# Kernel tuning notes

Hardware: AMD Instinct MI355X
Metric: run time of the kernel (lower is better)

Reference implementation:

```python
import jax, jax.numpy as jnp
import numpy as np

GRID_SIZE = 8
MARGIN = 1.0
EPS = 1e-8


def _centers_xy(hc, wc, gs):
    # pixel coordinates of cell centers for a hc x wc grid with stride gs, (x, y) order
    ys = jnp.arange(hc, dtype=jnp.float32) * gs + gs / 2.0 - 0.5
    xs = jnp.arange(wc, dtype=jnp.float32) * gs + gs / 2.0 - 0.5
    gy, gx = jnp.meshgrid(ys, xs, indexing='ij')
    return jnp.stack([gx, gy], axis=-1).reshape(-1, 2)  # (hc*wc, 2)


def _warp_xy(coords_xy, homo):
    # coords_xy: (n,2), homo: (b,3,3) -> (b,n,2) perspective warp
    p = jnp.concatenate([coords_xy, jnp.ones_like(coords_xy[..., :1])], axis=-1)  # (n,3)
    q = jnp.einsum('bij,nj->bni', homo, p)
    return q[..., :2] / (q[..., 2:3] + EPS)


def _bilinear(img, coords_yx):
    # img: (b,c,h,w); coords_yx: (b,n,2) pixel coords -> (b,n,c), zero padding outside
    b, c, h, w = img.shape
    y, x = coords_yx[..., 0], coords_yx[..., 1]
    y0, x0 = jnp.floor(y), jnp.floor(x)
    wy1, wx1 = y - y0, x - x0

    def gat(yi, xi):
        valid = (yi >= 0) & (yi <= h - 1) & (xi >= 0) & (xi <= w - 1)
        yc = jnp.clip(yi, 0, h - 1).astype(jnp.int32)
        xc = jnp.clip(xi, 0, w - 1).astype(jnp.int32)
        v = jax.vmap(lambda im, yy, xx: im[:, yy, xx].T)(img, yc, xc)  # (b,n,c)
        return v * valid[..., None].astype(img.dtype)

    return (gat(y0, x0) * ((1 - wy1) * (1 - wx1))[..., None]
            + gat(y0, x0 + 1) * ((1 - wy1) * wx1)[..., None]
            + gat(y0 + 1, x0) * (wy1 * (1 - wx1))[..., None]
            + gat(y0 + 1, x0 + 1) * (wy1 * wx1)[..., None])


def setup_inputs():
    key = jax.random.key(0)
    k = jax.random.split(key, 6)
    b, c, H, W = 2, 64, 480, 640
    hc, wc = H // GRID_SIZE, W // GRID_SIZE
    score1 = jax.random.uniform(k[0], (b, 1, H, W), dtype=jnp.float32)
    score2 = jax.random.uniform(k[1], (b, 1, H, W), dtype=jnp.float32)
    desc1 = jax.random.normal(k[2], (b, c, hc, wc), dtype=jnp.float32)
    desc1 = desc1 / jnp.linalg.norm(desc1, axis=1, keepdims=True)
    desc2 = jax.random.normal(k[3], (b, c, hc, wc), dtype=jnp.float32)
    desc2 = desc2 / jnp.linalg.norm(desc2, axis=1, keepdims=True)
    homo12 = jnp.eye(3, dtype=jnp.float32)[None] + 0.005 * jax.random.normal(k[4], (b, 3, 3), dtype=jnp.float32)
    homo21 = jnp.linalg.inv(homo12)
    return {"score1": score1, "score2": score2, "desc1": desc1, "desc2": desc2,
            "homo12": homo12, "homo21": homo21}


def reference(score1, score2, desc1, desc2, homo12, homo21):
    b, c, hc, wc = desc1.shape
    H, W = score1.shape[-2], score1.shape[-1]
    n = hc * wc
    gs = GRID_SIZE

    # warp image1 cell centers into image2 pixel space
    coo1_xy = _centers_xy(hc, wc, gs)                 # (n,2) x,y
    w_xy = _warp_xy(coo1_xy, homo12)                  # (b,n,2)
    w_yx = w_xy[..., ::-1]                            # (b,n,2) y,x

    # sample image2 descriptors at warped locations (desc-grid coordinates)
    d_yx = (w_yx - gs / 2.0 + 0.5) / gs
    w_desc1 = _bilinear(desc2, d_yx)                  # (b,n,c)
    w_desc1 = w_desc1 / (jnp.linalg.norm(w_desc1, axis=-1, keepdims=True) + EPS)

    # visibility: warp a ones image by homo21; keep only fully visible cells
    pix_xy = _centers_xy(H, W, 1)                     # (H*W,2)
    wp_xy = _warp_xy(pix_xy, homo21)                  # (b,HW,2)
    ones = jnp.ones((b, 1, H, W), desc1.dtype)
    vis = (_bilinear(ones, wp_xy[..., ::-1]) > 0).astype(desc1.dtype)  # (b,HW,1)
    vis = vis.reshape(b, 1, hc, gs, wc, gs).transpose(0, 3, 5, 1, 2, 4).reshape(b, gs * gs, hc, wc)
    w_vis_mask = jnp.prod(vis, axis=1).reshape(b, 1, n)

    # pairwise coordinate distances + 4-NN neighbor mask
    coo2_yx = _centers_xy(hc, wc, gs)[:, ::-1]        # (n,2) y,x
    a2 = jnp.sum(w_yx * w_yx, axis=-1)                # (b,n)
    b2 = jnp.sum(coo2_yx * coo2_yx, axis=-1)          # (n,)
    coo_dist = jnp.sqrt(jnp.clip(
        a2[:, :, None] + b2[None, None, :] - 2.0 * jnp.einsum('bnd,md->bnm', w_yx, coo2_yx), 0.0))
    _, ids = jax.lax.top_k(-coo_dist, 4)              # 4 smallest distances
    bi = jnp.arange(b)[:, None, None]
    ri = jnp.arange(n)[None, :, None]
    neigh_mask = jnp.zeros_like(coo_dist).at[bi, ri, ids].set(1.0)

    # descriptor inverse-similarity (euclidean distance of unit descriptors)
    d1 = desc1.reshape(b, c, n).transpose(0, 2, 1)    # (b,n,c)
    d2 = desc2.reshape(b, c, n).transpose(0, 2, 1)
    desc_sim = jnp.sqrt(jnp.clip(2.0 - 2.0 * jnp.einsum('bnc,bmc->bnm', d1, d2), EPS))
    desc_sim = desc_sim + neigh_mask * 5.0 + (1.0 - w_vis_mask) * 5.0

    # keypoints whose warps land inside image2
    in_b = ((w_yx[..., 0] >= 0) & (w_yx[..., 0] <= H - 1)
            & (w_yx[..., 1] >= 0) & (w_yx[..., 1] <= W - 1))
    match_mask = in_b.astype(desc1.dtype)             # (b,n)

    pos_sim = jnp.sqrt(jnp.clip(2.0 - 2.0 * jnp.sum(d1 * w_desc1, axis=-1), EPS))
    neg_sim = jnp.min(desc_sim, axis=-1)
    loss = jnp.clip(pos_sim - neg_sim + MARGIN, 0.0) ** 2
    return jnp.sum(loss * match_mask) / jnp.sum(match_mask)
```

## Files before the change

### kernel.cpp

```cpp
#include <hip/hip_runtime.h>
#include <math.h>

#define GS 8
#define HC 60
#define WC 80
#define NN 4800
#define CC 64
#define BB 2
#define HIMG 480
#define WIMG 640
#define EPSF 1e-8f
#define NCT 300
#define TGN 24
#define BIGF 1e30f

typedef __attribute__((ext_vector_type(8))) short short8v;
typedef __attribute__((ext_vector_type(4))) float f32x4;

__device__ __forceinline__ unsigned short f2bf(float f) {
    unsigned u = __float_as_uint(f);
    u += 0x7FFFu + ((u >> 16) & 1u);
    return (unsigned short)(u >> 16);
}

__global__ __launch_bounds__(256) void k_pre(
    const float* __restrict__ desc1, const float* __restrict__ desc2,
    const float* __restrict__ homo12, const float* __restrict__ homo21,
    unsigned short* __restrict__ d1bf, unsigned short* __restrict__ d2bf,
    float* __restrict__ posim, float* __restrict__ matchm,
    float* __restrict__ biasf, int* __restrict__ neighpk,
    unsigned int* __restrict__ negbits)
{
    __shared__ unsigned short tile[CC][65];
    int bid = blockIdx.x;
    int tid = threadIdx.x;

    if (bid < 2 * BB * 75) {
        int arr = bid / (BB * 75);
        int rem = bid % (BB * 75);
        int b = rem / 75;
        int t = rem % 75;
        int c0 = t * 64;
        const float* in = arr ? desc2 : desc1;
        unsigned short* out = arr ? d2bf : d1bf;
        int w = tid >> 6, l = tid & 63;
        #pragma unroll
        for (int k = 0; k < 16; k++) {
            int ch = k * 4 + w;
            tile[ch][l] = f2bf(in[((size_t)(b * CC + ch)) * NN + c0 + l]);
        }
        __syncthreads();
        #pragma unroll
        for (int k = 0; k < 16; k++) {
            int cell = k * 4 + w;
            out[((size_t)b * NN + c0 + cell) * CC + l] = tile[l][cell];
        }
        return;
    }

    int sub = bid - 2 * BB * 75;
    int wv = tid >> 6, lane = tid & 63;
    int idx = sub * 4 + wv;
    int b = idx / NN, r = idx - b * NN;
    int ci = r / WC, cj = r - ci * WC;

    int allv;
    {
        const float* h = homo21 + b * 9;
        int di = lane >> 3, dj = lane & 7;
        float y = (float)(ci * 8 + di);
        float x = (float)(cj * 8 + dj);
        float qx = h[0]*x + h[1]*y + h[2];
        float qy = h[3]*x + h[4]*y + h[5];
        float qw = h[6]*x + h[7]*y + h[8];
        float px = qx / (qw + EPSF);
        float py = qy / (qw + EPSF);
        float y0 = floorf(py), x0 = floorf(px);
        float ty = py - y0,   tx = px - x0;
        float fyv = ((y0 >= 0.0f && y0 <= (float)(HIMG-1)) ? (1.0f-ty) : 0.0f)
                  + ((y0+1.0f >= 0.0f && y0+1.0f <= (float)(HIMG-1)) ? ty : 0.0f);
        float fxv = ((x0 >= 0.0f && x0 <= (float)(WIMG-1)) ? (1.0f-tx) : 0.0f)
                  + ((x0+1.0f >= 0.0f && x0+1.0f <= (float)(WIMG-1)) ? tx : 0.0f);
        int ok = (fyv > 0.0f && fxv > 0.0f) ? 1 : 0;
        allv = __all(ok);
    }

    const float* h = homo12 + b * 9;
    float xx = cj * 8.0f + 3.5f;
    float yy = ci * 8.0f + 3.5f;
    float qx = h[0]*xx + h[1]*yy + h[2];
    float qy = h[3]*xx + h[4]*yy + h[5];
    float qw = h[6]*xx + h[7]*yy + h[8];
    float wx = qx / (qw + EPSF);
    float wy = qy / (qw + EPSF);
    float dy = (wy - 4.0f + 0.5f) / 8.0f;
    float dx = (wx - 4.0f + 0.5f) / 8.0f;

    float y0f = floorf(dy), x0f = floorf(dx);
    float fy = dy - y0f, fx = dx - x0f;
    float y1f = y0f + 1.0f, x1f = x0f + 1.0f;
    bool v0y = (y0f >= 0.0f && y0f <= (float)(HC-1));
    bool v1y = (y1f >= 0.0f && y1f <= (float)(HC-1));
    bool v0x = (x0f >= 0.0f && x0f <= (float)(WC-1));
    bool v1x = (x1f >= 0.0f && x1f <= (float)(WC-1));
    float w00 = (1.0f-fy)*(1.0f-fx); if (!(v0y && v0x)) w00 = 0.0f;
    float w01 = (1.0f-fy)*fx;        if (!(v0y && v1x)) w01 = 0.0f;
    float w10 = fy*(1.0f-fx);        if (!(v1y && v0x)) w10 = 0.0f;
    float w11 = fy*fx;               if (!(v1y && v1x)) w11 = 0.0f;
    int yc0 = (int)fminf(fmaxf(y0f, 0.0f), (float)(HC-1));
    int yc1 = (int)fminf(fmaxf(y1f, 0.0f), (float)(HC-1));
    int xc0 = (int)fminf(fmaxf(x0f, 0.0f), (float)(WC-1));
    int xc1 = (int)fminf(fmaxf(x1f, 0.0f), (float)(WC-1));
    int o00 = yc0*WC + xc0, o01 = yc0*WC + xc1;
    int o10 = yc1*WC + xc0, o11 = yc1*WC + xc1;

    int ch = lane;
    const float* d2b = desc2 + (size_t)b * CC * NN;
    const float* p = d2b + ch * NN;
    float wvl = w00*p[o00] + w01*p[o01] + w10*p[o10] + w11*p[o11];
    float s2 = wvl * wvl;
    float sd = desc1[((size_t)(b * CC + ch)) * NN + r] * wvl;
    #pragma unroll
    for (int off = 1; off < 64; off <<= 1) {
        s2 += __shfl_xor(s2, off);
        sd += __shfl_xor(sd, off);
    }

    if (lane == 0) {
        biasf[idx] = allv ? 16.0f : 8.0f;
        matchm[idx] = (wy >= 0.0f && wy <= (float)(HIMG-1) &&
                       wx >= 0.0f && wx <= (float)(WIMG-1)) ? 1.0f : 0.0f;
        float dot = sd / (sqrtf(s2) + EPSF);
        posim[idx] = sqrtf(fmaxf(2.0f - 2.0f*dot, EPSF));

        int i0 = (int)floorf(dy);
        int j0 = (int)floorf(dx);
        int ilo = i0 - 1; if (ilo < 0) ilo = 0; if (ilo > HC-4) ilo = HC-4;
        int jlo = j0 - 1; if (jlo < 0) jlo = 0; if (jlo > WC-4) jlo = WC-4;
        float bd0=3e38f, bd1=3e38f, bd2=3e38f, bd3=3e38f;
        int   id0=0,     id1=0,     id2=0,     id3=0;
        #pragma unroll
        for (int a = 0; a < 4; a++) {
            float cy = (float)(ilo + a) * 8.0f + 3.5f;
            float ddy = wy - cy;
            float ddy2 = ddy * ddy;
            #pragma unroll
            for (int q = 0; q < 4; q++) {
                float cx = (float)(jlo + q) * 8.0f + 3.5f;
                float ddx = wx - cx;
                float dv = ddy2 + ddx * ddx;
                int id = (ilo + a) * WC + (jlo + q);
                if (dv < bd3) {
                    bd3 = dv; id3 = id;
                    if (bd3 < bd2) { float tf=bd2; bd2=bd3; bd3=tf; int ti=id2; id2=id3; id3=ti; }
                    if (bd2 < bd1) { float tf=bd1; bd1=bd2; bd2=tf; int ti=id1; id1=id2; id2=ti; }
                    if (bd1 < bd0) { float tf=bd0; bd0=bd1; bd1=tf; int ti=id0; id0=id1; id1=ti; }
                }
            }
        }
        int base = ilo * WC + jlo;
        int mask = 0;
        {
            int d, ri, rj;
            d = id0 - base; ri = d / WC; rj = d - ri * WC; mask |= 1 << (ri*4+rj);
            d = id1 - base; ri = d / WC; rj = d - ri * WC; mask |= 1 << (ri*4+rj);
            d = id2 - base; ri = d / WC; rj = d - ri * WC; mask |= 1 << (ri*4+rj);
            d = id3 - base; ri = d / WC; rj = d - ri * WC; mask |= 1 << (ri*4+rj);
        }
        neighpk[idx] = mask | (ilo << 16) | (jlo << 24);
        negbits[idx] = 0x7F800000u;
    }
}


#define GLL(gp, lp) __builtin_amdgcn_global_load_lds(                        \
    (const __attribute__((address_space(1))) unsigned int*)(gp),             \
    (__attribute__((address_space(3))) unsigned int*)(lp), 16, 0, 0)

#define MFMA16(A, B, C) __builtin_amdgcn_mfma_f32_16x16x32_bf16((A), (B), (C), 0, 0, 0)

__global__ __launch_bounds__(64) void k_negmin(
    const unsigned short* __restrict__ d1bf, const unsigned short* __restrict__ d2bf,
    const float* __restrict__ biasf, const int* __restrict__ neighpk,
    unsigned int* __restrict__ negbits)
{
    __shared__ unsigned short Bsm[2][1024];

    int bid = blockIdx.x;
    int b   = bid / (150 * TGN);
    int rem = bid % (150 * TGN);
    int rb  = rem / TGN;
    int tg  = rem % TGN;
    int lane = threadIdx.x;
    int l15 = lane & 15, lg = lane >> 4;
    int r0  = rb * 32;
    int wl  = l15;
    int lg8 = lg * 8;
    int bNN = b * NN;

    const unsigned short* d1b = d1bf + (size_t)bNN * CC;
    const unsigned short* d2b = d2bf + (size_t)bNN * CC;

    short8v afr00 = *(const short8v*)(d1b + (size_t)(r0 + l15) * CC + lg8);
    short8v afr01 = *(const short8v*)(d1b + (size_t)(r0 + l15) * CC + 32 + lg8);
    short8v afr10 = *(const short8v*)(d1b + (size_t)(r0 + 16 + l15) * CC + lg8);
    short8v afr11 = *(const short8v*)(d1b + (size_t)(r0 + 16 + l15) * CC + 32 + lg8);

    int pk[8];
    int lmin = 0x7FFFFFFF, lmax = -1;
    #pragma unroll
    for (int s_ = 0; s_ < 8; s_++) {
        int row = r0 + (s_ >> 2) * 16 + lg * 4 + (s_ & 3);
        int p = neighpk[bNN + row];
        pk[s_] = p;
        int ilo = (p >> 16) & 0xFF, jlo = (p >> 24) & 0xFF;
        int idm = ilo * WC + jlo;
        lmin = min(lmin, idm);
        lmax = max(lmax, idm + 3 * WC + 3);
    }
    #pragma unroll
    for (int off = 1; off < 64; off <<= 1) {
        lmin = min(lmin, __shfl_xor(lmin, off));
        lmax = max(lmax, __shfl_xor(lmax, off));
    }

    float m[8];
    #pragma unroll
    for (int i = 0; i < 8; i++) m[i] = -BIGF;

    int o0 = lane;
    int o1 = lane + 64;
    int s0 = (o0 & ~7) | ((o0 ^ (o0 >> 3)) & 7);
    int s1 = (o1 & ~7) | ((o1 ^ (o1 >> 3)) & 7);

    int nt = (NCT - tg + TGN - 1) / TGN;

    {
        const unsigned short* tb0 = d2b + (size_t)(tg * 16) * CC;
        GLL(tb0 + s0 * 8, &Bsm[0][0]);
        GLL(tb0 + s1 * 8, &Bsm[0][512]);
    }
    float bias = biasf[bNN + tg * 16 + wl];
    __syncthreads();

    int buf = 0;
    for (int it = 0; it < nt; it++) {
        int t = tg + it * TGN;

        float bias_n = 0.0f;
        if (it + 1 < nt) {
            const unsigned short* tbn = d2b + (size_t)((t + TGN) * 16) * CC;
            GLL(tbn + s0 * 8, &Bsm[buf ^ 1][0]);
            GLL(tbn + s1 * 8, &Bsm[buf ^ 1][512]);
            bias_n = biasf[bNN + (t + TGN) * 16 + wl];
        }

        const unsigned short* lb = &Bsm[buf][0];
        short8v b0 = *(const short8v*)(lb + (size_t)wl * 64 + (size_t)((lg ^ wl) & 7) * 8);
        short8v b1 = *(const short8v*)(lb + (size_t)wl * 64 + (size_t)(((4 + lg) ^ wl) & 7) * 8);

        f32x4 a0 = {bias, bias, bias, bias};
        f32x4 a1 = a0;
        a0 = MFMA16(afr00, b0, a0);
        a0 = MFMA16(afr01, b1, a0);
        a1 = MFMA16(afr10, b0, a1);
        a1 = MFMA16(afr11, b1, a1);

        int tb = t * 16;
        if (tb + 15 < lmin || tb > lmax) {
            #pragma unroll
            for (int g_ = 0; g_ < 4; g_++) {
                m[g_]   = fmaxf(m[g_],   a0[g_]);
                m[4+g_] = fmaxf(m[4+g_], a1[g_]);
            }
        } else {
            int c_ = tb + wl;
            int gi_ = c_ / WC; int gj_ = c_ - gi_ * WC;
            #pragma unroll
            for (int s_ = 0; s_ < 8; s_++) {
                int p_ = pk[s_]; int msk_ = p_ & 0xFFFF;
                unsigned ri_ = (unsigned)(gi_ - ((p_ >> 16) & 0xFF));
                unsigned rj_ = (unsigned)(gj_ - ((p_ >> 24) & 0xFF));
                unsigned bx_ = (ri_ < 4u && rj_ < 4u) ? (ri_ * 4u + rj_) : 16u;
                bool nb_ = ((msk_ >> bx_) & 1) != 0;
                float sv_ = (s_ < 4) ? a0[s_ & 3] : a1[s_ & 3];
                float key_ = nb_ ? sv_ - 8.0f : sv_;
                m[s_] = fmaxf(m[s_], key_);
            }
        }

        bias = bias_n;
        buf ^= 1;
        __syncthreads();
    }

    #pragma unroll
    for (int s_ = 0; s_ < 8; s_++) {
        float mv = m[s_];
        float pen, sdot;
        if (mv >= 12.0f)     { pen = 0.0f;  sdot = mv - 16.0f; }
        else if (mv >= 4.0f) { pen = 5.0f;  sdot = mv - 8.0f; }
        else                 { pen = 10.0f; sdot = mv; }
        float res = sqrtf(fmaxf(2.0f - 2.0f * sdot, EPSF)) + pen;
        #pragma unroll
        for (int off = 1; off < 16; off <<= 1)
            res = fminf(res, __shfl_xor(res, off));
        if (l15 == 0) {
            int row = r0 + (s_ >> 2) * 16 + lg * 4 + (s_ & 3);
            atomicMin(&negbits[bNN + row], __float_as_uint(res));
        }
    }
}

__global__ void k_loss(const float* __restrict__ posim, const float* __restrict__ matchm,
                       const unsigned int* __restrict__ negbits, float* __restrict__ bpart)
{
    __shared__ float sn[256], sdn[256];
    int tid = threadIdx.x;
    int idx = blockIdx.x * 256 + tid;
    float num = 0.0f, den = 0.0f;
    if (idx < BB * NN) {
        float neg = __uint_as_float(negbits[idx]);
        float l = fmaxf(posim[idx] - neg + 1.0f, 0.0f);
        float mm = matchm[idx];
        num = l * l * mm;
        den = mm;
    }
    sn[tid] = num; sdn[tid] = den;
    __syncthreads();
    for (int st = 128; st > 0; st >>= 1) {
        if (tid < st) { sn[tid] += sn[tid + st]; sdn[tid] += sdn[tid + st]; }
        __syncthreads();
    }
    if (tid == 0) { bpart[blockIdx.x * 2] = sn[0]; bpart[blockIdx.x * 2 + 1] = sdn[0]; }
}

__global__ void k_sum(const float* __restrict__ bpart, int nb, float* __restrict__ out)
{
    int t = threadIdx.x;
    float num = 0.0f, den = 0.0f;
    if (t < nb) { num = bpart[t * 2]; den = bpart[t * 2 + 1]; }
    #pragma unroll
    for (int off = 1; off < 64; off <<= 1) {
        num += __shfl_xor(num, off);
        den += __shfl_xor(den, off);
    }
    if (t == 0) out[0] = num / den;
}

extern "C" void kernel_launch(void* const* d_in, const int* in_sizes, int n_in,
                              void* d_out, int out_size, void* d_ws, size_t ws_size,
                              hipStream_t stream)
{
    const float* desc1  = (const float*)d_in[2];
    const float* desc2  = (const float*)d_in[3];
    const float* homo12 = (const float*)d_in[4];
    const float* homo21 = (const float*)d_in[5];
    float* out = (float*)d_out;

    float*        biasf   = (float*)d_ws;
    float*        posim   = biasf + BB * NN;
    float*        matchm  = posim + BB * NN;
    int*          neighpk = (int*)(matchm + BB * NN);
    unsigned int* negbits = (unsigned int*)(neighpk + BB * NN);
    float*        bpart   = (float*)(negbits + BB * NN);
    unsigned short* d1bf  = (unsigned short*)(bpart + 128);
    unsigned short* d2bf  = d1bf + (size_t)BB * NN * CC;

    int nb = (BB * NN + 255) / 256;
    int nb_pre = 2 * BB * 75 + 2 * BB * 75 * 4;
    k_pre<<<nb_pre, 256, 0, stream>>>(desc1, desc2, homo12, homo21,
                                      d1bf, d2bf, posim, matchm, biasf, neighpk, negbits);
    k_negmin<<<BB * 150 * TGN, 64, 0, stream>>>(d1bf, d2bf, biasf, neighpk, negbits);
    k_loss<<<nb, 256, 0, stream>>>(posim, matchm, negbits, bpart);
    k_sum<<<1, 64, 0, stream>>>(bpart, nb, out);
}
```

Before: 38.76 us.

## Triple-buffer descriptor tiles with explicit vmcnt waits, staging bias through LDS

Replaces the double-buffered loop, which called __syncthreads every iteration, with a three-stage ring. Descriptor tiles and bias values are prefetched two iterations ahead using global_load_lds, and the loop waits on explicit s_waitcnt vmcnt counts instead of a barrier. Bias now moves through LDS via 4-byte DMA loads instead of per-lane register prefetch. This hides more global-load latency for the single-wave blocks, but it relies on hand-counted vmcnt values and uses extra LDS, so any miscount could read a tile before it has arrived.

```diff
diff --git a/kernel.cpp b/kernel.cpp
--- a/kernel.cpp
+++ b/kernel.cpp
@@ -173,9 +173,12 @@
 }
 
 
-#define GLL(gp, lp) __builtin_amdgcn_global_load_lds(                        \
+#define GLL16(gp, lp) __builtin_amdgcn_global_load_lds(                      \
     (const __attribute__((address_space(1))) unsigned int*)(gp),             \
     (__attribute__((address_space(3))) unsigned int*)(lp), 16, 0, 0)
+#define GLL4(gp, lp) __builtin_amdgcn_global_load_lds(                       \
+    (const __attribute__((address_space(1))) unsigned int*)(gp),             \
+    (__attribute__((address_space(3))) unsigned int*)(lp), 4, 0, 0)
 
 #define MFMA16(A, B, C) __builtin_amdgcn_mfma_f32_16x16x32_bf16((A), (B), (C), 0, 0, 0)
 
@@ -184,7 +187,8 @@
     const float* __restrict__ biasf, const int* __restrict__ neighpk,
     unsigned int* __restrict__ negbits)
 {
-    __shared__ unsigned short Bsm[2][1024];
+    __shared__ unsigned short Bsm[3][1024];
+    __shared__ float Bias[3][64];
 
     int bid = blockIdx.x;
     int b   = bid / (150 * TGN);
@@ -235,64 +239,64 @@
 
     int nt = (NCT - tg + TGN - 1) / TGN;
 
-    {
-        const unsigned short* tb0 = d2b + (size_t)(tg * 16) * CC;
-        GLL(tb0 + s0 * 8, &Bsm[0][0]);
-        GLL(tb0 + s1 * 8, &Bsm[0][512]);
-    }
-    float bias = biasf[bNN + tg * 16 + wl];
-    __syncthreads();
-
-    int buf = 0;
-    for (int it = 0; it < nt; it++) {
-        int t = tg + it * TGN;
-
-        float bias_n = 0.0f;
-        if (it + 1 < nt) {
-            const unsigned short* tbn = d2b + (size_t)((t + TGN) * 16) * CC;
-            GLL(tbn + s0 * 8, &Bsm[buf ^ 1][0]);
-            GLL(tbn + s1 * 8, &Bsm[buf ^ 1][512]);
-            bias_n = biasf[bNN + (t + TGN) * 16 + wl];
-        }
-
-        const unsigned short* lb = &Bsm[buf][0];
-        short8v b0 = *(const short8v*)(lb + (size_t)wl * 64 + (size_t)((lg ^ wl) & 7) * 8);
-        short8v b1 = *(const short8v*)(lb + (size_t)wl * 64 + (size_t)(((4 + lg) ^ wl) & 7) * 8);
-
-        f32x4 a0 = {bias, bias, bias, bias};
-        f32x4 a1 = a0;
-        a0 = MFMA16(afr00, b0, a0);
-        a0 = MFMA16(afr01, b1, a0);
-        a1 = MFMA16(afr10, b0, a1);
-        a1 = MFMA16(afr11, b1, a1);
-
-        int tb = t * 16;
-        if (tb + 15 < lmin || tb > lmax) {
-            #pragma unroll
-            for (int g_ = 0; g_ < 4; g_++) {
-                m[g_]   = fmaxf(m[g_],   a0[g_]);
-                m[4+g_] = fmaxf(m[4+g_], a1[g_]);
-            }
-        } else {
-            int c_ = tb + wl;
-            int gi_ = c_ / WC; int gj_ = c_ - gi_ * WC;
-            #pragma unroll
-            for (int s_ = 0; s_ < 8; s_++) {
-                int p_ = pk[s_]; int msk_ = p_ & 0xFFFF;
-                unsigned ri_ = (unsigned)(gi_ - ((p_ >> 16) & 0xFF));
-                unsigned rj_ = (unsigned)(gj_ - ((p_ >> 24) & 0xFF));
-                unsigned bx_ = (ri_ < 4u && rj_ < 4u) ? (ri_ * 4u + rj_) : 16u;
-                bool nb_ = ((msk_ >> bx_) & 1) != 0;
-                float sv_ = (s_ < 4) ? a0[s_ & 3] : a1[s_ & 3];
-                float key_ = nb_ ? sv_ - 8.0f : sv_;
-                m[s_] = fmaxf(m[s_], key_);
-            }
-        }
-
-        bias = bias_n;
-        buf ^= 1;
-        __syncthreads();
-    }
+#define STAGE(T, S) do {                                                     \
+    const unsigned short* tbp_ = d2b + (size_t)((T) * 16) * CC;              \
+    GLL16(tbp_ + s0 * 8, &Bsm[S][0]);                                        \
+    GLL16(tbp_ + s1 * 8, &Bsm[S][512]);                                      \
+    GLL4(biasf + bNN + (T) * 16 + l15, &Bias[S][0]);                         \
+} while (0)
+
+#define COMP(T, S) do {                                                      \
+    const unsigned short* lb_ = &Bsm[S][0];                                  \
+    short8v b0_ = *(const short8v*)(lb_ + (size_t)wl * 64 +                  \
+                                    (size_t)((lg ^ wl) & 7) * 8);            \
+    short8v b1_ = *(const short8v*)(lb_ + (size_t)wl * 64 +                  \
+                                    (size_t)(((4 + lg) ^ wl) & 7) * 8);      \
+    float bi_ = Bias[S][wl];                                                 \
+    f32x4 a0_ = {bi_, bi_, bi_, bi_};                                        \
+    f32x4 a1_ = a0_;                                                         \
+    a0_ = MFMA16(afr00, b0_, a0_);                                           \
+    a0_ = MFMA16(afr01, b1_, a0_);                                           \
+    a1_ = MFMA16(afr10, b0_, a1_);                                           \
+    a1_ = MFMA16(afr11, b1_, a1_);                                           \
+    int tb_ = (T) * 16;                                                      \
+    if (tb_ + 15 < lmin || tb_ > lmax) {                                     \
+        _Pragma("unroll")                                                    \
+        for (int g_ = 0; g_ < 4; g_++) {                                     \
+            m[g_]   = fmaxf(m[g_],   a0_[g_]);                               \
+            m[4+g_] = fmaxf(m[4+g_], a1_[g_]);                               \
+        }                                                                    \
+    } else {                                                                 \
+        int c_ = tb_ + wl;                                                   \
+        int gi_ = c_ / WC; int gj_ = c_ - gi_ * WC;                          \
+        _Pragma("unroll")                                                    \
+        for (int s_ = 0; s_ < 8; s_++) {                                     \
+            int p_ = pk[s_]; int msk_ = p_ & 0xFFFF;                         \
+            unsigned ri_ = (unsigned)(gi_ - ((p_ >> 16) & 0xFF));            \
+            unsigned rj_ = (unsigned)(gj_ - ((p_ >> 24) & 0xFF));            \
+            unsigned bx_ = (ri_ < 4u && rj_ < 4u) ? (ri_ * 4u + rj_) : 16u;  \
+            bool nb_ = ((msk_ >> bx_) & 1) != 0;                             \
+            float sv_ = (s_ < 4) ? a0_[s_ & 3] : a1_[s_ & 3];                \
+            float key_ = nb_ ? sv_ - 8.0f : sv_;                             \
+            m[s_] = fmaxf(m[s_], key_);                                      \
+        }                                                                    \
+    }                                                                        \
+} while (0)
+
+    STAGE(tg, 0);
+    STAGE(tg + TGN, 1);
+
+    int it = 0;
+    for (; it + 2 < nt; it++) {
+        STAGE(tg + (it + 2) * TGN, (it + 2) % 3);
+        asm volatile("s_waitcnt vmcnt(6)" ::: "memory");
+        COMP(tg + it * TGN, it % 3);
+    }
+    asm volatile("s_waitcnt vmcnt(3)" ::: "memory");
+    COMP(tg + it * TGN, it % 3);
+    it++;
+    asm volatile("s_waitcnt vmcnt(0)" ::: "memory");
+    COMP(tg + it * TGN, it % 3);
 
     #pragma unroll
     for (int s_ = 0; s_ < 8; s_++) {
```

Measured after the change: 41.45 us. 1.07x slower.
